# Kernel tuning notes

Hardware: AMD Instinct MI355X
Metric: run time of the kernel (lower is better)

## Reference

```python
import jax, jax.numpy as jnp
import numpy as np

ORDER = 3
OS_FACTOR = 1.5
B, T, I, H = 32, 1024, 512, 512

def _lagrange_kernel(order, os_factor):
    # mirrors LagrangeInterp_RNN.__init__
    if os_factor >= 2:
        delta = os_factor - np.floor(os_factor) + 1
    else:
        delta = os_factor - 1
    k = np.ones(order + 1, dtype=np.float64)
    for n in range(order + 1):
        for j in range(order + 1):
            if j != n:
                k[n] *= (delta - j) / (n - j)
    return jnp.asarray(k, dtype=jnp.float32)

def setup_inputs() -> dict:
    key = jax.random.key(0)
    k1, k2, k3, k4, k5 = jax.random.split(key, 5)
    s = 1.0 / np.sqrt(H)
    return {
        "x": jax.random.normal(k1, (B, T, I), dtype=jnp.float32),
        "Wih": jax.random.uniform(k2, (H, I), minval=-s, maxval=s, dtype=jnp.float32),
        "Whh": jax.random.uniform(k3, (H, H), minval=-s, maxval=s, dtype=jnp.float32),
        "bih": jax.random.uniform(k4, (H,), minval=-s, maxval=s, dtype=jnp.float32),
        "bhh": jax.random.uniform(k5, (H,), minval=-s, maxval=s, dtype=jnp.float32),
        "kernel": _lagrange_kernel(ORDER, OS_FACTOR),
    }

def reference(x, Wih, Whh, bih, bhh, kernel):
    # x: [B, T, I]; kernel: [order+1]; prev_states: [B, order+1, H]
    b = x.shape[0]
    h_dim = Whh.shape[0]
    prev0 = jnp.zeros((b, kernel.shape[0], h_dim), dtype=x.dtype)
    # input projection is independent of the recurrence -> one big GEMM
    xproj = jnp.einsum('bti,hi->bth', x, Wih) + bih  # [B, T, H]

    def step(prev, xp_t):
        # Lagrange-interpolated read of the history window
        h_read = jnp.einsum('k,bkh->bh', kernel, prev)
        h = jnp.tanh(xp_t + h_read @ Whh.T + bhh)
        # torch code detaches the state stored into prev_states, then rolls
        # so the newest (detached) state sits at index 0 (epsilon == 1)
        new_prev = jnp.concatenate(
            [jax.lax.stop_gradient(h)[:, None, :], prev[:, :-1, :]], axis=1)
        return new_prev, h

    _, states_t = jax.lax.scan(step, prev0, jnp.swapaxes(xproj, 0, 1))
    states = jnp.swapaxes(states_t, 0, 1)  # [B, T, H]
    return states, states[:, -1, :]
```

## Files before the change

kernel.cpp:

```cpp
#include <hip/hip_runtime.h>

typedef __bf16 bf16x8 __attribute__((ext_vector_type(8)));
typedef float  f32x4  __attribute__((ext_vector_type(4)));
typedef unsigned long long u64;

#define AGENT __HIP_MEMORY_SCOPE_AGENT

__device__ __forceinline__ float fast_tanh(float x) {
    float e = __expf(2.0f * x);
    return 1.0f - 2.0f * __builtin_amdgcn_rcpf(e + 1.0f);
}

__device__ __forceinline__ void lds_barrier() {
    asm volatile("s_waitcnt lgkmcnt(0)" ::: "memory");
    __builtin_amdgcn_s_barrier();
}

__global__ __launch_bounds__(256) void xproj_gemm_kernel(
    const float* __restrict__ x, const float* __restrict__ Wih,
    const float* __restrict__ bih, float* __restrict__ out)
{
    __shared__ __bf16 Ash[64][72];
    __shared__ __bf16 Bsh[64][72];

    const int tid  = threadIdx.x;
    const int wave = tid >> 6, lane = tid & 63;
    const int col  = lane & 15, kq = lane >> 4;
    const int bt0  = blockIdx.x * 64;
    const int h0   = blockIdx.y * 64;

    f32x4 acc[4];
#pragma unroll
    for (int nt = 0; nt < 4; ++nt) acc[nt] = (f32x4){0.f, 0.f, 0.f, 0.f};

    const int r  = tid >> 2;
    const int cb = (tid & 3) * 16;

    for (int k0 = 0; k0 < 512; k0 += 64) {
        const float* ax = x   + (size_t)(bt0 + r) * 512 + k0 + cb;
        const float* bx = Wih + (size_t)(h0  + r) * 512 + k0 + cb;
#pragma unroll
        for (int j = 0; j < 4; ++j) {
            const float4 av = ((const float4*)ax)[j];
            const float4 bv = ((const float4*)bx)[j];
            const int c = cb + 4 * j;
            Ash[r][c+0]=(__bf16)av.x; Ash[r][c+1]=(__bf16)av.y;
            Ash[r][c+2]=(__bf16)av.z; Ash[r][c+3]=(__bf16)av.w;
            Bsh[r][c+0]=(__bf16)bv.x; Bsh[r][c+1]=(__bf16)bv.y;
            Bsh[r][c+2]=(__bf16)bv.z; Bsh[r][c+3]=(__bf16)bv.w;
        }
        __syncthreads();
#pragma unroll
        for (int kt = 0; kt < 2; ++kt) {
            bf16x8 a = *(const bf16x8*)&Ash[wave * 16 + col][kt * 32 + kq * 8];
#pragma unroll
            for (int nt = 0; nt < 4; ++nt) {
                bf16x8 bb = *(const bf16x8*)&Bsh[nt * 16 + col][kt * 32 + kq * 8];
                acc[nt] = __builtin_amdgcn_mfma_f32_16x16x32_bf16(a, bb, acc[nt], 0, 0, 0);
            }
        }
        __syncthreads();
    }
#pragma unroll
    for (int nt = 0; nt < 4; ++nt) {
        const float bv = bih[h0 + nt * 16 + col];
#pragma unroll
        for (int reg = 0; reg < 4; ++reg) {
            const int m = bt0 + wave * 16 + kq * 4 + reg;
            out[(size_t)m * 512 + h0 + nt * 16 + col] = acc[nt][reg] + bv;
        }
    }
}

__global__ __launch_bounds__(256) void lagrange_rnn_kernel(
    const float* __restrict__ Whh, const float* __restrict__ bhh,
    const float* __restrict__ kern, float* __restrict__ out,
    u64* __restrict__ mbox)
{
    const int id   = blockIdx.x;
    const int b    = (id & 7) + ((id >> 5) << 3);
    const int p    = (id >> 3) & 3;
    const int tid  = threadIdx.x;
    const int wave = tid >> 6, lane = tid & 63;
    const int col  = lane & 15, kq = lane >> 4;

    __shared__ float  hist[4][512];
    __shared__ __bf16 hread[2][512];

    for (int i = tid; i < 2048; i += 256) ((float*)hist)[i] = 0.f;
    for (int i = tid; i < 512;  i += 256) { hread[0][i] = (__bf16)0.f; hread[1][i] = (__bf16)0.f; }

    const int hA = p * 128 + wave * 32 + col;
    const int hB = hA + 16;
    bf16x8 wf0[16], wf1[16];
#pragma unroll
    for (int j = 0; j < 16; ++j) {
        const int ktg = ((j + 4 * p) & 15) * 32 + kq * 8;
        const float* s0 = Whh + (size_t)hA * 512 + ktg;
        const float* s1 = Whh + (size_t)hB * 512 + ktg;
        const float4 a0 = *(const float4*)s0, a1 = *(const float4*)(s0 + 4);
        const float4 b0 = *(const float4*)s1, b1 = *(const float4*)(s1 + 4);
        bf16x8 w;
        w[0]=(__bf16)a0.x; w[1]=(__bf16)a0.y; w[2]=(__bf16)a0.z; w[3]=(__bf16)a0.w;
        w[4]=(__bf16)a1.x; w[5]=(__bf16)a1.y; w[6]=(__bf16)a1.z; w[7]=(__bf16)a1.w;
        wf0[j] = w;
        w[0]=(__bf16)b0.x; w[1]=(__bf16)b0.y; w[2]=(__bf16)b0.z; w[3]=(__bf16)b0.w;
        w[4]=(__bf16)b1.x; w[5]=(__bf16)b1.y; w[6]=(__bf16)b1.z; w[7]=(__bf16)b1.w;
        wf1[j] = w;
    }
    const float k0 = kern[0], k1 = kern[1], k2 = kern[2], k3 = kern[3];
    const float bA = bhh[hA], bB = bhh[hB];
    float* stA = out + (size_t)b * 1024 * 512 + hA;
    const int peer = (p + wave) & 3;
    const int j0 = peer * 128 + lane * 2;
    const bool comp = (lane < 16);
    const int abase = p * 128 + kq * 8;

    float xA = 0.f, xB = 0.f;
    __syncthreads();
    if (comp) { xA = stA[0]; xB = stA[16]; }

    for (int t = 0; t < 1024; ++t) {
        const int rb = t & 1, wb = rb ^ 1;
        const int rt = t & 3;
        const int rm1 = (t + 3) & 3, rm2 = (t + 2) & 3, rm3 = (t + 1) & 3;
        const u64* mb_peer = mbox + (size_t)(((b << 1) | rb) * 4 + peer) * 128;
        const bool polling = (t != 0) && (wave != 0);
        const unsigned want = (unsigned)t;

        float nxA = 0.f, nxB = 0.f;
        if (comp) {
            nxA = stA[(size_t)(t + 1) * 512];
            nxB = stA[(size_t)(t + 1) * 512 + 16];
        }
        u64 v0 = 0, v1 = 0;
        if (polling) {
            v0 = __hip_atomic_load(&mb_peer[lane * 2],     __ATOMIC_RELAXED, AGENT);
            v1 = __hip_atomic_load(&mb_peer[lane * 2 + 1], __ATOMIC_RELAXED, AGENT);
        }

        lds_barrier();

        f32x4 acc0 = (f32x4){0,0,0,0}, acc1 = (f32x4){0,0,0,0};
#pragma unroll
        for (int j = 0; j < 4; ++j) {
            bf16x8 a = *(const bf16x8*)&hread[rb][(abase + 32 * j) & 511];
            acc0 = __builtin_amdgcn_mfma_f32_16x16x32_bf16(a, wf0[j], acc0, 0, 0, 0);
            acc1 = __builtin_amdgcn_mfma_f32_16x16x32_bf16(a, wf1[j], acc1, 0, 0, 0);
        }

        if (polling) {
            while ((unsigned)(v0 >> 32) != want || (unsigned)(v1 >> 32) != want) {
                v0 = __hip_atomic_load(&mb_peer[lane * 2],     __ATOMIC_RELAXED, AGENT);
                v1 = __hip_atomic_load(&mb_peer[lane * 2 + 1], __ATOMIC_RELAXED, AGENT);
            }
            union { unsigned u; float f; } d0, d1;
            d0.u = (unsigned)v0; d1.u = (unsigned)v1;
            const float q0 = k1 * hist[rm2][j0]     + k2 * hist[rm3][j0]     + k3 * hist[rt][j0];
            const float q1 = k1 * hist[rm2][j0 + 1] + k2 * hist[rm3][j0 + 1] + k3 * hist[rt][j0 + 1];
            hread[rb][j0]     = (__bf16)(q0 + k0 * d0.f);
            hread[rb][j0 + 1] = (__bf16)(q1 + k0 * d1.f);
            hist[rm1][j0]     = d0.f;
            hist[rm1][j0 + 1] = d1.f;
        }

        lds_barrier();

        float ppA = 0.f, ppB = 0.f;
        if (comp) {
            ppA = k1 * hist[rm1][hA] + k2 * hist[rm2][hA] + k3 * hist[rm3][hA];
            ppB = k1 * hist[rm1][hB] + k2 * hist[rm2][hB] + k3 * hist[rm3][hB];
        }

        f32x4 c0a = (f32x4){0,0,0,0}, c0b = (f32x4){0,0,0,0}, c0c = (f32x4){0,0,0,0};
        f32x4 c1a = (f32x4){0,0,0,0}, c1b = (f32x4){0,0,0,0}, c1c = (f32x4){0,0,0,0};
#pragma unroll
        for (int j = 4; j < 8; ++j) {
            bf16x8 a = *(const bf16x8*)&hread[rb][(abase + 32 * j) & 511];
            c0a = __builtin_amdgcn_mfma_f32_16x16x32_bf16(a, wf0[j], c0a, 0, 0, 0);
            c1a = __builtin_amdgcn_mfma_f32_16x16x32_bf16(a, wf1[j], c1a, 0, 0, 0);
        }
#pragma unroll
        for (int j = 8; j < 12; ++j) {
            bf16x8 a = *(const bf16x8*)&hread[rb][(abase + 32 * j) & 511];
            c0b = __builtin_amdgcn_mfma_f32_16x16x32_bf16(a, wf0[j], c0b, 0, 0, 0);
            c1b = __builtin_amdgcn_mfma_f32_16x16x32_bf16(a, wf1[j], c1b, 0, 0, 0);
        }
#pragma unroll
        for (int j = 12; j < 16; ++j) {
            bf16x8 a = *(const bf16x8*)&hread[rb][(abase + 32 * j) & 511];
            c0c = __builtin_amdgcn_mfma_f32_16x16x32_bf16(a, wf0[j], c0c, 0, 0, 0);
            c1c = __builtin_amdgcn_mfma_f32_16x16x32_bf16(a, wf1[j], c1c, 0, 0, 0);
        }

        if (comp) {
            const float hAv = fast_tanh(xA + acc0[0] + c0a[0] + c0b[0] + c0c[0] + bA);
            const float hBv = fast_tanh(xB + acc1[0] + c1a[0] + c1b[0] + c1c[0] + bB);
            u64* mb_self = mbox + (size_t)(((b << 1) | wb) * 4 + p) * 128;
            const u64 tag = (u64)(unsigned)(t + 1) << 32;
            union { float f; unsigned u; } cA, cB;
            cA.f = hAv; cB.f = hBv;
            __hip_atomic_store(&mb_self[wave * 32 + col],      tag | cA.u, __ATOMIC_RELAXED, AGENT);
            __hip_atomic_store(&mb_self[wave * 32 + col + 16], tag | cB.u, __ATOMIC_RELAXED, AGENT);
            stA[(size_t)t * 512]      = hAv;
            stA[(size_t)t * 512 + 16] = hBv;
            hist[rt][hA] = hAv;  hread[wb][hA] = (__bf16)(ppA + k0 * hAv);
            hist[rt][hB] = hBv;  hread[wb][hB] = (__bf16)(ppB + k0 * hBv);
        }
        xA = nxA; xB = nxB;
    }

    float* out2 = out + (size_t)32 * 1024 * 512 + (size_t)b * 512;
    if (comp) {
        out2[hA] = hist[3][hA];
        out2[hB] = hist[3][hB];
    }
}

extern "C" void kernel_launch(void* const* d_in, const int* in_sizes, int n_in,
                              void* d_out, int out_size, void* d_ws, size_t ws_size,
                              hipStream_t stream) {
    const float* x    = (const float*)d_in[0];
    const float* Wih  = (const float*)d_in[1];
    const float* Whh  = (const float*)d_in[2];
    const float* bih  = (const float*)d_in[3];
    const float* bhh  = (const float*)d_in[4];
    const float* kern = (const float*)d_in[5];
    float* out = (float*)d_out;

    u64* mbox = (u64*)d_ws;

    dim3 g1(512, 8, 1);
    xproj_gemm_kernel<<<g1, 256, 0, stream>>>(x, Wih, bih, out);
    lagrange_rnn_kernel<<<128, 256, 0, stream>>>(Whh, bhh, kern, out, mbox);
}
```

Baseline: 1.301 ms.

## Split mailbox into fast local-scope poll path with agent-scope fallback republish

Inter-block exchange of hidden state now goes through two mailboxes. Compute lanes write with plain volatile stores to a local mailbox. Pollers read it with an sc0 dwordx4 asm load and, after 16 spins, fall back to an agent-scope mailbox that wave 0 republishes each step from LDS history. Next-step xproj prefetch moves to wave 0 and is staged through a double-buffered LDS array. The aim is lower latency on the cross-block handshake, at the cost of relying on cache-scope visibility semantics, which risks stale reads or extra spin traffic.

```diff
diff --git a/kernel.cpp b/kernel.cpp
--- a/kernel.cpp
+++ b/kernel.cpp
@@ -3,6 +3,7 @@
 typedef __bf16 bf16x8 __attribute__((ext_vector_type(8)));
 typedef float  f32x4  __attribute__((ext_vector_type(4)));
 typedef unsigned long long u64;
+typedef u64 u64x2 __attribute__((ext_vector_type(2)));
 
 #define AGENT __HIP_MEMORY_SCOPE_AGENT
 
@@ -14,6 +15,14 @@
 __device__ __forceinline__ void lds_barrier() {
     asm volatile("s_waitcnt lgkmcnt(0)" ::: "memory");
     __builtin_amdgcn_s_barrier();
+}
+
+__device__ __forceinline__ u64x2 poll_ld(const u64* p) {
+    u64x2 v;
+    asm volatile("global_load_dwordx4 %0, %1, off sc0\n\t"
+                 "s_waitcnt vmcnt(0)"
+                 : "=v"(v) : "v"(p));
+    return v;
 }
 
 __global__ __launch_bounds__(256) void xproj_gemm_kernel(
@@ -75,7 +84,7 @@
 __global__ __launch_bounds__(256) void lagrange_rnn_kernel(
     const float* __restrict__ Whh, const float* __restrict__ bhh,
     const float* __restrict__ kern, float* __restrict__ out,
-    u64* __restrict__ mbox)
+    u64* __restrict__ mboxG, u64* __restrict__ mboxL)
 {
     const int id   = blockIdx.x;
     const int b    = (id & 7) + ((id >> 5) << 3);
@@ -86,6 +95,7 @@
 
     __shared__ float  hist[4][512];
     __shared__ __bf16 hread[2][512];
+    __shared__ float  xpb[2][128];
 
     for (int i = tid; i < 2048; i += 256) ((float*)hist)[i] = 0.f;
     for (int i = tid; i < 512;  i += 256) { hread[0][i] = (__bf16)0.f; hread[1][i] = (__bf16)0.f; }
@@ -111,33 +121,26 @@
     const float k0 = kern[0], k1 = kern[1], k2 = kern[2], k3 = kern[3];
     const float bA = bhh[hA], bB = bhh[hB];
     float* stA = out + (size_t)b * 1024 * 512 + hA;
+    const float* xsrc = out + (size_t)b * 1024 * 512 + p * 128 + lane * 2;
     const int peer = (p + wave) & 3;
     const int j0 = peer * 128 + lane * 2;
     const bool comp = (lane < 16);
     const int abase = p * 128 + kq * 8;
-
-    float xA = 0.f, xB = 0.f;
+    const int xslot = wave * 32 + col;
+
+    if (wave == 0) {
+        const float2 x0 = *(const float2*)xsrc;
+        xpb[0][lane * 2] = x0.x; xpb[0][lane * 2 + 1] = x0.y;
+    }
     __syncthreads();
-    if (comp) { xA = stA[0]; xB = stA[16]; }
 
     for (int t = 0; t < 1024; ++t) {
         const int rb = t & 1, wb = rb ^ 1;
         const int rt = t & 3;
         const int rm1 = (t + 3) & 3, rm2 = (t + 2) & 3, rm3 = (t + 1) & 3;
-        const u64* mb_peer = mbox + (size_t)(((b << 1) | rb) * 4 + peer) * 128;
-        const bool polling = (t != 0) && (wave != 0);
-        const unsigned want = (unsigned)t;
-
-        float nxA = 0.f, nxB = 0.f;
-        if (comp) {
-            nxA = stA[(size_t)(t + 1) * 512];
-            nxB = stA[(size_t)(t + 1) * 512 + 16];
-        }
-        u64 v0 = 0, v1 = 0;
-        if (polling) {
-            v0 = __hip_atomic_load(&mb_peer[lane * 2],     __ATOMIC_RELAXED, AGENT);
-            v1 = __hip_atomic_load(&mb_peer[lane * 2 + 1], __ATOMIC_RELAXED, AGENT);
-        }
+
+        float2 nx = {0.f, 0.f};
+        if (wave == 0) nx = *(const float2*)(xsrc + (size_t)(t + 1) * 512);
 
         lds_barrier();
 
@@ -149,13 +152,32 @@
             acc1 = __builtin_amdgcn_mfma_f32_16x16x32_bf16(a, wf1[j], acc1, 0, 0, 0);
         }
 
-        if (polling) {
-            while ((unsigned)(v0 >> 32) != want || (unsigned)(v1 >> 32) != want) {
-                v0 = __hip_atomic_load(&mb_peer[lane * 2],     __ATOMIC_RELAXED, AGENT);
-                v1 = __hip_atomic_load(&mb_peer[lane * 2 + 1], __ATOMIC_RELAXED, AGENT);
+        if (wave == 0) {
+            u64* mg = mboxG + (size_t)(((b << 1) | rb) * 4 + p) * 128;
+            union { float f; unsigned u; } a0, a1;
+            a0.f = hist[rm1][p * 128 + lane * 2];
+            a1.f = hist[rm1][p * 128 + lane * 2 + 1];
+            const u64 tg = (u64)(unsigned)t << 32;
+            __hip_atomic_store(&mg[lane * 2],     tg | a0.u, __ATOMIC_RELAXED, AGENT);
+            __hip_atomic_store(&mg[lane * 2 + 1], tg | a1.u, __ATOMIC_RELAXED, AGENT);
+        } else if (t) {
+            const unsigned want = (unsigned)t;
+            const u64* ml = mboxL + (size_t)(((b << 1) | rb) * 4 + peer) * 128 + lane * 2;
+            const u64* mg = mboxG + (size_t)(((b << 1) | rb) * 4 + peer) * 128 + lane * 2;
+            u64x2 v = poll_ld(ml);
+            int spins = 0;
+            while ((unsigned)(v[0] >> 32) != want || (unsigned)(v[1] >> 32) != want) {
+                if (++spins > 16) {
+                    const u64 g0 = __hip_atomic_load(&mg[0], __ATOMIC_RELAXED, AGENT);
+                    const u64 g1 = __hip_atomic_load(&mg[1], __ATOMIC_RELAXED, AGENT);
+                    if ((unsigned)(g0 >> 32) == want && (unsigned)(g1 >> 32) == want) {
+                        v[0] = g0; v[1] = g1; break;
+                    }
+                }
+                v = poll_ld(ml);
             }
             union { unsigned u; float f; } d0, d1;
-            d0.u = (unsigned)v0; d1.u = (unsigned)v1;
+            d0.u = (unsigned)v[0]; d1.u = (unsigned)v[1];
             const float q0 = k1 * hist[rm2][j0]     + k2 * hist[rm3][j0]     + k3 * hist[rt][j0];
             const float q1 = k1 * hist[rm2][j0 + 1] + k2 * hist[rm3][j0 + 1] + k3 * hist[rt][j0 + 1];
             hread[rb][j0]     = (__bf16)(q0 + k0 * d0.f);
@@ -166,8 +188,10 @@
 
         lds_barrier();
 
-        float ppA = 0.f, ppB = 0.f;
+        float xAv = 0.f, xBv = 0.f, ppA = 0.f, ppB = 0.f;
         if (comp) {
+            xAv = xpb[rb][xslot];
+            xBv = xpb[rb][xslot + 16];
             ppA = k1 * hist[rm1][hA] + k2 * hist[rm2][hA] + k3 * hist[rm3][hA];
             ppB = k1 * hist[rm1][hB] + k2 * hist[rm2][hB] + k3 * hist[rm3][hB];
         }
@@ -194,20 +218,23 @@
         }
 
         if (comp) {
-            const float hAv = fast_tanh(xA + acc0[0] + c0a[0] + c0b[0] + c0c[0] + bA);
-            const float hBv = fast_tanh(xB + acc1[0] + c1a[0] + c1b[0] + c1c[0] + bB);
-            u64* mb_self = mbox + (size_t)(((b << 1) | wb) * 4 + p) * 128;
+            const float hAv = fast_tanh(xAv + acc0[0] + c0a[0] + c0b[0] + c0c[0] + bA);
+            const float hBv = fast_tanh(xBv + acc1[0] + c1a[0] + c1b[0] + c1c[0] + bB);
+            volatile u64* ms = (volatile u64*)(mboxL + (size_t)(((b << 1) | wb) * 4 + p) * 128);
             const u64 tag = (u64)(unsigned)(t + 1) << 32;
             union { float f; unsigned u; } cA, cB;
             cA.f = hAv; cB.f = hBv;
-            __hip_atomic_store(&mb_self[wave * 32 + col],      tag | cA.u, __ATOMIC_RELAXED, AGENT);
-            __hip_atomic_store(&mb_self[wave * 32 + col + 16], tag | cB.u, __ATOMIC_RELAXED, AGENT);
+            ms[wave * 32 + col]      = tag | cA.u;
+            ms[wave * 32 + col + 16] = tag | cB.u;
             stA[(size_t)t * 512]      = hAv;
             stA[(size_t)t * 512 + 16] = hBv;
             hist[rt][hA] = hAv;  hread[wb][hA] = (__bf16)(ppA + k0 * hAv);
             hist[rt][hB] = hBv;  hread[wb][hB] = (__bf16)(ppB + k0 * hBv);
         }
-        xA = nxA; xB = nxB;
+        if (wave == 0) {
+            xpb[wb][lane * 2]     = nx.x;
+            xpb[wb][lane * 2 + 1] = nx.y;
+        }
     }
 
     float* out2 = out + (size_t)32 * 1024 * 512 + (size_t)b * 512;
@@ -228,9 +255,10 @@
     const float* kern = (const float*)d_in[5];
     float* out = (float*)d_out;
 
-    u64* mbox = (u64*)d_ws;
+    u64* mboxG = (u64*)d_ws;
+    u64* mboxL = mboxG + 32 * 2 * 4 * 128;
 
     dim3 g1(512, 8, 1);
     xproj_gemm_kernel<<<g1, 256, 0, stream>>>(x, Wih, bih, out);
-    lagrange_rnn_kernel<<<128, 256, 0, stream>>>(Whh, bhh, kern, out, mbox);
-}
+    lagrange_rnn_kernel<<<128, 256, 0, stream>>>(Whh, bhh, kern, out, mboxG, mboxL);
+}
```

New measurement: 4.473 ms. 3.44x slower.

## Interleave two batch recurrences per block to hide cross-block mailbox latency

Applied to the files above, without the earlier changes.

Each block now handles two batch rows instead of one, alternating between them within every timestep, and the grid shrinks from 128 to 64 blocks. While one batch waits on its peer mailbox, the other batch's MFMA work runs, and mailbox loads are prefetched one phase early. The next step's input projection is staged through LDS by wave 0. The aim is to hide inter-block polling latency on the serial critical path. The cost is twice the work per block per step, more barriers and more LDS use.

```diff
diff --git a/kernel.cpp b/kernel.cpp
--- a/kernel.cpp
+++ b/kernel.cpp
@@ -5,6 +5,7 @@
 typedef unsigned long long u64;
 
 #define AGENT __HIP_MEMORY_SCOPE_AGENT
+#define MFMA  __builtin_amdgcn_mfma_f32_16x16x32_bf16
 
 __device__ __forceinline__ float fast_tanh(float x) {
     float e = __expf(2.0f * x);
@@ -56,7 +57,7 @@
 #pragma unroll
             for (int nt = 0; nt < 4; ++nt) {
                 bf16x8 bb = *(const bf16x8*)&Bsh[nt * 16 + col][kt * 32 + kq * 8];
-                acc[nt] = __builtin_amdgcn_mfma_f32_16x16x32_bf16(a, bb, acc[nt], 0, 0, 0);
+                acc[nt] = MFMA(a, bb, acc[nt], 0, 0, 0);
             }
         }
         __syncthreads();
@@ -78,17 +79,19 @@
     u64* __restrict__ mbox)
 {
     const int id   = blockIdx.x;
-    const int b    = (id & 7) + ((id >> 5) << 3);
-    const int p    = (id >> 3) & 3;
+    const int p    = id & 3;
+    const int q    = id >> 2;
+    const int b0   = q * 2, b1 = q * 2 + 1;
     const int tid  = threadIdx.x;
     const int wave = tid >> 6, lane = tid & 63;
     const int col  = lane & 15, kq = lane >> 4;
 
-    __shared__ float  hist[4][512];
-    __shared__ __bf16 hread[2][512];
-
-    for (int i = tid; i < 2048; i += 256) ((float*)hist)[i] = 0.f;
-    for (int i = tid; i < 512;  i += 256) { hread[0][i] = (__bf16)0.f; hread[1][i] = (__bf16)0.f; }
+    __shared__ float  hist[2][4][512];
+    __shared__ __bf16 hread[2][2][512];
+    __shared__ float  xpb[2][2][128];
+
+    for (int i = tid; i < 4096; i += 256) ((float*)hist)[i] = 0.f;
+    for (int i = tid; i < 2048; i += 256) ((__bf16*)hread)[i] = (__bf16)0.f;
 
     const int hA = p * 128 + wave * 32 + col;
     const int hB = hA + 16;
@@ -99,121 +102,214 @@
         const float* s0 = Whh + (size_t)hA * 512 + ktg;
         const float* s1 = Whh + (size_t)hB * 512 + ktg;
         const float4 a0 = *(const float4*)s0, a1 = *(const float4*)(s0 + 4);
-        const float4 b0 = *(const float4*)s1, b1 = *(const float4*)(s1 + 4);
+        const float4 c0 = *(const float4*)s1, c1 = *(const float4*)(s1 + 4);
         bf16x8 w;
         w[0]=(__bf16)a0.x; w[1]=(__bf16)a0.y; w[2]=(__bf16)a0.z; w[3]=(__bf16)a0.w;
         w[4]=(__bf16)a1.x; w[5]=(__bf16)a1.y; w[6]=(__bf16)a1.z; w[7]=(__bf16)a1.w;
         wf0[j] = w;
-        w[0]=(__bf16)b0.x; w[1]=(__bf16)b0.y; w[2]=(__bf16)b0.z; w[3]=(__bf16)b0.w;
-        w[4]=(__bf16)b1.x; w[5]=(__bf16)b1.y; w[6]=(__bf16)b1.z; w[7]=(__bf16)b1.w;
+        w[0]=(__bf16)c0.x; w[1]=(__bf16)c0.y; w[2]=(__bf16)c0.z; w[3]=(__bf16)c0.w;
+        w[4]=(__bf16)c1.x; w[5]=(__bf16)c1.y; w[6]=(__bf16)c1.z; w[7]=(__bf16)c1.w;
         wf1[j] = w;
     }
     const float k0 = kern[0], k1 = kern[1], k2 = kern[2], k3 = kern[3];
     const float bA = bhh[hA], bB = bhh[hB];
-    float* stA = out + (size_t)b * 1024 * 512 + hA;
+    float* st0 = out + (size_t)b0 * 1024 * 512 + hA;
+    float* st1 = out + (size_t)b1 * 1024 * 512 + hA;
+    const float* xs0 = out + (size_t)b0 * 1024 * 512 + p * 128 + lane * 2;
+    const float* xs1 = out + (size_t)b1 * 1024 * 512 + p * 128 + lane * 2;
     const int peer = (p + wave) & 3;
     const int j0 = peer * 128 + lane * 2;
     const bool comp = (lane < 16);
     const int abase = p * 128 + kq * 8;
-
-    float xA = 0.f, xB = 0.f;
+    const int xslot = wave * 32 + col;
+
+    if (wave == 0) {
+        const float2 x0 = *(const float2*)xs0;
+        const float2 x1 = *(const float2*)xs1;
+        xpb[0][0][lane * 2] = x0.x; xpb[0][0][lane * 2 + 1] = x0.y;
+        xpb[1][0][lane * 2] = x1.x; xpb[1][0][lane * 2 + 1] = x1.y;
+    }
     __syncthreads();
-    if (comp) { xA = stA[0]; xB = stA[16]; }
+
+    u64 pva0 = 0, pva1 = 0;
+    u64 pvb0 = 0, pvb1 = 0;
 
     for (int t = 0; t < 1024; ++t) {
         const int rb = t & 1, wb = rb ^ 1;
         const int rt = t & 3;
         const int rm1 = (t + 3) & 3, rm2 = (t + 2) & 3, rm3 = (t + 1) & 3;
-        const u64* mb_peer = mbox + (size_t)(((b << 1) | rb) * 4 + peer) * 128;
-        const bool polling = (t != 0) && (wave != 0);
         const unsigned want = (unsigned)t;
 
-        float nxA = 0.f, nxB = 0.f;
-        if (comp) {
-            nxA = stA[(size_t)(t + 1) * 512];
-            nxB = stA[(size_t)(t + 1) * 512 + 16];
-        }
-        u64 v0 = 0, v1 = 0;
-        if (polling) {
-            v0 = __hip_atomic_load(&mb_peer[lane * 2],     __ATOMIC_RELAXED, AGENT);
-            v1 = __hip_atomic_load(&mb_peer[lane * 2 + 1], __ATOMIC_RELAXED, AGENT);
+        float2 nx0 = {0.f, 0.f}, nx1 = {0.f, 0.f};
+        if (wave == 0) {
+            nx0 = *(const float2*)(xs0 + (size_t)(t + 1) * 512);
+            nx1 = *(const float2*)(xs1 + (size_t)(t + 1) * 512);
         }
 
         lds_barrier();
-
         f32x4 acc0 = (f32x4){0,0,0,0}, acc1 = (f32x4){0,0,0,0};
 #pragma unroll
         for (int j = 0; j < 4; ++j) {
-            bf16x8 a = *(const bf16x8*)&hread[rb][(abase + 32 * j) & 511];
-            acc0 = __builtin_amdgcn_mfma_f32_16x16x32_bf16(a, wf0[j], acc0, 0, 0, 0);
-            acc1 = __builtin_amdgcn_mfma_f32_16x16x32_bf16(a, wf1[j], acc1, 0, 0, 0);
-        }
-
-        if (polling) {
-            while ((unsigned)(v0 >> 32) != want || (unsigned)(v1 >> 32) != want) {
-                v0 = __hip_atomic_load(&mb_peer[lane * 2],     __ATOMIC_RELAXED, AGENT);
-                v1 = __hip_atomic_load(&mb_peer[lane * 2 + 1], __ATOMIC_RELAXED, AGENT);
+            bf16x8 a = *(const bf16x8*)&hread[0][rb][(abase + 32 * j) & 511];
+            acc0 = MFMA(a, wf0[j], acc0, 0, 0, 0);
+            acc1 = MFMA(a, wf1[j], acc1, 0, 0, 0);
+        }
+        if (wave != 0 && t) {
+            u64 v0 = pva0, v1 = pva1;
+            if ((unsigned)(v0 >> 32) != want || (unsigned)(v1 >> 32) != want) {
+                const u64* mg = mbox + (size_t)(((b0 << 1) | rb) * 4 + peer) * 128 + lane * 2;
+                do {
+                    v0 = __hip_atomic_load(&mg[0], __ATOMIC_RELAXED, AGENT);
+                    v1 = __hip_atomic_load(&mg[1], __ATOMIC_RELAXED, AGENT);
+                } while ((unsigned)(v0 >> 32) != want || (unsigned)(v1 >> 32) != want);
             }
             union { unsigned u; float f; } d0, d1;
             d0.u = (unsigned)v0; d1.u = (unsigned)v1;
-            const float q0 = k1 * hist[rm2][j0]     + k2 * hist[rm3][j0]     + k3 * hist[rt][j0];
-            const float q1 = k1 * hist[rm2][j0 + 1] + k2 * hist[rm3][j0 + 1] + k3 * hist[rt][j0 + 1];
-            hread[rb][j0]     = (__bf16)(q0 + k0 * d0.f);
-            hread[rb][j0 + 1] = (__bf16)(q1 + k0 * d1.f);
-            hist[rm1][j0]     = d0.f;
-            hist[rm1][j0 + 1] = d1.f;
-        }
-
+            const float q0 = k1 * hist[0][rm2][j0]     + k2 * hist[0][rm3][j0]     + k3 * hist[0][rt][j0];
+            const float q1 = k1 * hist[0][rm2][j0 + 1] + k2 * hist[0][rm3][j0 + 1] + k3 * hist[0][rt][j0 + 1];
+            hread[0][rb][j0]     = (__bf16)(q0 + k0 * d0.f);
+            hread[0][rb][j0 + 1] = (__bf16)(q1 + k0 * d1.f);
+            hist[0][rm1][j0]     = d0.f;
+            hist[0][rm1][j0 + 1] = d1.f;
+        }
         lds_barrier();
-
-        float ppA = 0.f, ppB = 0.f;
+        if (wave != 0 && t) {
+            const u64* mg = mbox + (size_t)(((b1 << 1) | rb) * 4 + peer) * 128 + lane * 2;
+            pvb0 = __hip_atomic_load(&mg[0], __ATOMIC_RELAXED, AGENT);
+            pvb1 = __hip_atomic_load(&mg[1], __ATOMIC_RELAXED, AGENT);
+        }
+        float xAv = 0.f, xBv = 0.f, ppA = 0.f, ppB = 0.f;
         if (comp) {
-            ppA = k1 * hist[rm1][hA] + k2 * hist[rm2][hA] + k3 * hist[rm3][hA];
-            ppB = k1 * hist[rm1][hB] + k2 * hist[rm2][hB] + k3 * hist[rm3][hB];
-        }
-
+            xAv = xpb[0][rb][xslot];
+            xBv = xpb[0][rb][xslot + 16];
+            ppA = k1 * hist[0][rm1][hA] + k2 * hist[0][rm2][hA] + k3 * hist[0][rm3][hA];
+            ppB = k1 * hist[0][rm1][hB] + k2 * hist[0][rm2][hB] + k3 * hist[0][rm3][hB];
+        }
         f32x4 c0a = (f32x4){0,0,0,0}, c0b = (f32x4){0,0,0,0}, c0c = (f32x4){0,0,0,0};
         f32x4 c1a = (f32x4){0,0,0,0}, c1b = (f32x4){0,0,0,0}, c1c = (f32x4){0,0,0,0};
 #pragma unroll
         for (int j = 4; j < 8; ++j) {
-            bf16x8 a = *(const bf16x8*)&hread[rb][(abase + 32 * j) & 511];
-            c0a = __builtin_amdgcn_mfma_f32_16x16x32_bf16(a, wf0[j], c0a, 0, 0, 0);
-            c1a = __builtin_amdgcn_mfma_f32_16x16x32_bf16(a, wf1[j], c1a, 0, 0, 0);
+            bf16x8 a = *(const bf16x8*)&hread[0][rb][(abase + 32 * j) & 511];
+            c0a = MFMA(a, wf0[j], c0a, 0, 0, 0);
+            c1a = MFMA(a, wf1[j], c1a, 0, 0, 0);
         }
 #pragma unroll
         for (int j = 8; j < 12; ++j) {
-            bf16x8 a = *(const bf16x8*)&hread[rb][(abase + 32 * j) & 511];
-            c0b = __builtin_amdgcn_mfma_f32_16x16x32_bf16(a, wf0[j], c0b, 0, 0, 0);
-            c1b = __builtin_amdgcn_mfma_f32_16x16x32_bf16(a, wf1[j], c1b, 0, 0, 0);
+            bf16x8 a = *(const bf16x8*)&hread[0][rb][(abase + 32 * j) & 511];
+            c0b = MFMA(a, wf0[j], c0b, 0, 0, 0);
+            c1b = MFMA(a, wf1[j], c1b, 0, 0, 0);
         }
 #pragma unroll
         for (int j = 12; j < 16; ++j) {
-            bf16x8 a = *(const bf16x8*)&hread[rb][(abase + 32 * j) & 511];
-            c0c = __builtin_amdgcn_mfma_f32_16x16x32_bf16(a, wf0[j], c0c, 0, 0, 0);
-            c1c = __builtin_amdgcn_mfma_f32_16x16x32_bf16(a, wf1[j], c1c, 0, 0, 0);
-        }
-
+            bf16x8 a = *(const bf16x8*)&hread[0][rb][(abase + 32 * j) & 511];
+            c0c = MFMA(a, wf0[j], c0c, 0, 0, 0);
+            c1c = MFMA(a, wf1[j], c1c, 0, 0, 0);
+        }
         if (comp) {
-            const float hAv = fast_tanh(xA + acc0[0] + c0a[0] + c0b[0] + c0c[0] + bA);
-            const float hBv = fast_tanh(xB + acc1[0] + c1a[0] + c1b[0] + c1c[0] + bB);
-            u64* mb_self = mbox + (size_t)(((b << 1) | wb) * 4 + p) * 128;
+            const float hAv = fast_tanh(xAv + acc0[0] + c0a[0] + c0b[0] + c0c[0] + bA);
+            const float hBv = fast_tanh(xBv + acc1[0] + c1a[0] + c1b[0] + c1c[0] + bB);
+            u64* ms = mbox + (size_t)(((b0 << 1) | wb) * 4 + p) * 128;
             const u64 tag = (u64)(unsigned)(t + 1) << 32;
             union { float f; unsigned u; } cA, cB;
             cA.f = hAv; cB.f = hBv;
-            __hip_atomic_store(&mb_self[wave * 32 + col],      tag | cA.u, __ATOMIC_RELAXED, AGENT);
-            __hip_atomic_store(&mb_self[wave * 32 + col + 16], tag | cB.u, __ATOMIC_RELAXED, AGENT);
-            stA[(size_t)t * 512]      = hAv;
-            stA[(size_t)t * 512 + 16] = hBv;
-            hist[rt][hA] = hAv;  hread[wb][hA] = (__bf16)(ppA + k0 * hAv);
-            hist[rt][hB] = hBv;  hread[wb][hB] = (__bf16)(ppB + k0 * hBv);
-        }
-        xA = nxA; xB = nxB;
-    }
-
-    float* out2 = out + (size_t)32 * 1024 * 512 + (size_t)b * 512;
+            __hip_atomic_store(&ms[wave * 32 + col],      tag | cA.u, __ATOMIC_RELAXED, AGENT);
+            __hip_atomic_store(&ms[wave * 32 + col + 16], tag | cB.u, __ATOMIC_RELAXED, AGENT);
+            st0[(size_t)t * 512]      = hAv;
+            st0[(size_t)t * 512 + 16] = hBv;
+            hist[0][rt][hA] = hAv;  hread[0][wb][hA] = (__bf16)(ppA + k0 * hAv);
+            hist[0][rt][hB] = hBv;  hread[0][wb][hB] = (__bf16)(ppB + k0 * hBv);
+        }
+        if (wave == 0) {
+            xpb[0][wb][lane * 2]     = nx0.x;
+            xpb[0][wb][lane * 2 + 1] = nx0.y;
+        }
+
+        lds_barrier();
+        f32x4 e0 = (f32x4){0,0,0,0}, e1 = (f32x4){0,0,0,0};
+#pragma unroll
+        for (int j = 0; j < 4; ++j) {
+            bf16x8 a = *(const bf16x8*)&hread[1][rb][(abase + 32 * j) & 511];
+            e0 = MFMA(a, wf0[j], e0, 0, 0, 0);
+            e1 = MFMA(a, wf1[j], e1, 0, 0, 0);
+        }
+        if (wave != 0 && t) {
+            u64 v0 = pvb0, v1 = pvb1;
+            if ((unsigned)(v0 >> 32) != want || (unsigned)(v1 >> 32) != want) {
+                const u64* mg = mbox + (size_t)(((b1 << 1) | rb) * 4 + peer) * 128 + lane * 2;
+                do {
+                    v0 = __hip_atomic_load(&mg[0], __ATOMIC_RELAXED, AGENT);
+                    v1 = __hip_atomic_load(&mg[1], __ATOMIC_RELAXED, AGENT);
+                } while ((unsigned)(v0 >> 32) != want || (unsigned)(v1 >> 32) != want);
+            }
+            union { unsigned u; float f; } d0, d1;
+            d0.u = (unsigned)v0; d1.u = (unsigned)v1;
+            const float q0 = k1 * hist[1][rm2][j0]     + k2 * hist[1][rm3][j0]     + k3 * hist[1][rt][j0];
+            const float q1 = k1 * hist[1][rm2][j0 + 1] + k2 * hist[1][rm3][j0 + 1] + k3 * hist[1][rt][j0 + 1];
+            hread[1][rb][j0]     = (__bf16)(q0 + k0 * d0.f);
+            hread[1][rb][j0 + 1] = (__bf16)(q1 + k0 * d1.f);
+            hist[1][rm1][j0]     = d0.f;
+            hist[1][rm1][j0 + 1] = d1.f;
+        }
+        lds_barrier();
+        if (wave != 0) {
+            const u64* mg = mbox + (size_t)(((b0 << 1) | wb) * 4 + peer) * 128 + lane * 2;
+            pva0 = __hip_atomic_load(&mg[0], __ATOMIC_RELAXED, AGENT);
+            pva1 = __hip_atomic_load(&mg[1], __ATOMIC_RELAXED, AGENT);
+        }
+        float yAv = 0.f, yBv = 0.f, qpA = 0.f, qpB = 0.f;
+        if (comp) {
+            yAv = xpb[1][rb][xslot];
+            yBv = xpb[1][rb][xslot + 16];
+            qpA = k1 * hist[1][rm1][hA] + k2 * hist[1][rm2][hA] + k3 * hist[1][rm3][hA];
+            qpB = k1 * hist[1][rm1][hB] + k2 * hist[1][rm2][hB] + k3 * hist[1][rm3][hB];
+        }
+        f32x4 g0a = (f32x4){0,0,0,0}, g0b = (f32x4){0,0,0,0}, g0c = (f32x4){0,0,0,0};
+        f32x4 g1a = (f32x4){0,0,0,0}, g1b = (f32x4){0,0,0,0}, g1c = (f32x4){0,0,0,0};
+#pragma unroll
+        for (int j = 4; j < 8; ++j) {
+            bf16x8 a = *(const bf16x8*)&hread[1][rb][(abase + 32 * j) & 511];
+            g0a = MFMA(a, wf0[j], g0a, 0, 0, 0);
+            g1a = MFMA(a, wf1[j], g1a, 0, 0, 0);
+        }
+#pragma unroll
+        for (int j = 8; j < 12; ++j) {
+            bf16x8 a = *(const bf16x8*)&hread[1][rb][(abase + 32 * j) & 511];
+            g0b = MFMA(a, wf0[j], g0b, 0, 0, 0);
+            g1b = MFMA(a, wf1[j], g1b, 0, 0, 0);
+        }
+#pragma unroll
+        for (int j = 12; j < 16; ++j) {
+            bf16x8 a = *(const bf16x8*)&hread[1][rb][(abase + 32 * j) & 511];
+            g0c = MFMA(a, wf0[j], g0c, 0, 0, 0);
+            g1c = MFMA(a, wf1[j], g1c, 0, 0, 0);
+        }
+        if (comp) {
+            const float hAv = fast_tanh(yAv + e0[0] + g0a[0] + g0b[0] + g0c[0] + bA);
+            const float hBv = fast_tanh(yBv + e1[0] + g1a[0] + g1b[0] + g1c[0] + bB);
+            u64* ms = mbox + (size_t)(((b1 << 1) | wb) * 4 + p) * 128;
+            const u64 tag = (u64)(unsigned)(t + 1) << 32;
+            union { float f; unsigned u; } cA, cB;
+            cA.f = hAv; cB.f = hBv;
+            __hip_atomic_store(&ms[wave * 32 + col],      tag | cA.u, __ATOMIC_RELAXED, AGENT);
+            __hip_atomic_store(&ms[wave * 32 + col + 16], tag | cB.u, __ATOMIC_RELAXED, AGENT);
+            st1[(size_t)t * 512]      = hAv;
+            st1[(size_t)t * 512 + 16] = hBv;
+            hist[1][rt][hA] = hAv;  hread[1][wb][hA] = (__bf16)(qpA + k0 * hAv);
+            hist[1][rt][hB] = hBv;  hread[1][wb][hB] = (__bf16)(qpB + k0 * hBv);
+        }
+        if (wave == 0) {
+            xpb[1][wb][lane * 2]     = nx1.x;
+            xpb[1][wb][lane * 2 + 1] = nx1.y;
+        }
+    }
+
+    float* o0 = out + (size_t)32 * 1024 * 512 + (size_t)b0 * 512;
+    float* o1 = out + (size_t)32 * 1024 * 512 + (size_t)b1 * 512;
     if (comp) {
-        out2[hA] = hist[3][hA];
-        out2[hB] = hist[3][hB];
+        o0[hA] = hist[0][3][hA];
+        o0[hB] = hist[0][3][hB];
+        o1[hA] = hist[1][3][hA];
+        o1[hB] = hist[1][3][hB];
     }
 }
 
@@ -232,5 +328,5 @@
 
     dim3 g1(512, 8, 1);
     xproj_gemm_kernel<<<g1, 256, 0, stream>>>(x, Wih, bih, out);
-    lagrange_rnn_kernel<<<128, 256, 0, stream>>>(Whh, bhh, kern, out, mbox);
-}
+    lagrange_rnn_kernel<<<64, 256, 0, stream>>>(Whh, bhh, kern, out, mbox);
+}
```

After: 2.745 ms. +110.9%, slower.

## Batch 16 sequences per recurrent MFMA tile and exchange interpolated bf16 state

Applied to the files above, without the earlier changes.

The recurrent kernel now processes 16 batch rows per group of 4 blocks, so the MFMA M dimension carries real batch rows instead of one broadcast vector. The grid drops from 128 to 8 blocks. Peers exchange the already Lagrange-interpolated state as packed bf16 pairs through the mailbox, and history is kept in registers instead of LDS. bhh is folded into the input-projection bias. The cost is that only 8 CUs run the serial recurrence, each with more work per step and more mailbox traffic per thread.

```diff
diff --git a/kernel.cpp b/kernel.cpp
--- a/kernel.cpp
+++ b/kernel.cpp
@@ -5,6 +5,7 @@
 typedef unsigned long long u64;
 
 #define AGENT __HIP_MEMORY_SCOPE_AGENT
+#define MFMA  __builtin_amdgcn_mfma_f32_16x16x32_bf16
 
 __device__ __forceinline__ float fast_tanh(float x) {
     float e = __expf(2.0f * x);
@@ -18,7 +19,8 @@
 
 __global__ __launch_bounds__(256) void xproj_gemm_kernel(
     const float* __restrict__ x, const float* __restrict__ Wih,
-    const float* __restrict__ bih, float* __restrict__ out)
+    const float* __restrict__ bih, const float* __restrict__ bhh,
+    float* __restrict__ out)
 {
     __shared__ __bf16 Ash[64][72];
     __shared__ __bf16 Bsh[64][72];
@@ -56,164 +58,195 @@
 #pragma unroll
             for (int nt = 0; nt < 4; ++nt) {
                 bf16x8 bb = *(const bf16x8*)&Bsh[nt * 16 + col][kt * 32 + kq * 8];
-                acc[nt] = __builtin_amdgcn_mfma_f32_16x16x32_bf16(a, bb, acc[nt], 0, 0, 0);
+                acc[nt] = MFMA(a, bb, acc[nt], 0, 0, 0);
             }
         }
         __syncthreads();
     }
 #pragma unroll
     for (int nt = 0; nt < 4; ++nt) {
-        const float bv = bih[h0 + nt * 16 + col];
+        const int n = h0 + nt * 16 + col;
+        const float bv = bih[n] + bhh[n];
 #pragma unroll
         for (int reg = 0; reg < 4; ++reg) {
             const int m = bt0 + wave * 16 + kq * 4 + reg;
-            out[(size_t)m * 512 + h0 + nt * 16 + col] = acc[nt][reg] + bv;
-        }
-    }
-}
-
-__global__ __launch_bounds__(256) void lagrange_rnn_kernel(
-    const float* __restrict__ Whh, const float* __restrict__ bhh,
-    const float* __restrict__ kern, float* __restrict__ out,
-    u64* __restrict__ mbox)
+            out[(size_t)m * 512 + n] = acc[nt][reg] + bv;
+        }
+    }
+}
+
+#define TT  1024
+#define LDA 520
+
+__global__ __launch_bounds__(256, 1) void lagrange_rnn_kernel(
+    const float* __restrict__ Whh, const float* __restrict__ kern,
+    float* __restrict__ out, u64* __restrict__ mbox)
 {
     const int id   = blockIdx.x;
-    const int b    = (id & 7) + ((id >> 5) << 3);
-    const int p    = (id >> 3) & 3;
+    const int g    = id >> 2;
+    const int p    = id & 3;
     const int tid  = threadIdx.x;
-    const int wave = tid >> 6, lane = tid & 63;
+    const int w    = tid >> 6, lane = tid & 63;
     const int col  = lane & 15, kq = lane >> 4;
 
-    __shared__ float  hist[4][512];
-    __shared__ __bf16 hread[2][512];
-
-    for (int i = tid; i < 2048; i += 256) ((float*)hist)[i] = 0.f;
-    for (int i = tid; i < 512;  i += 256) { hread[0][i] = (__bf16)0.f; hread[1][i] = (__bf16)0.f; }
-
-    const int hA = p * 128 + wave * 32 + col;
-    const int hB = hA + 16;
-    bf16x8 wf0[16], wf1[16];
-#pragma unroll
-    for (int j = 0; j < 16; ++j) {
-        const int ktg = ((j + 4 * p) & 15) * 32 + kq * 8;
-        const float* s0 = Whh + (size_t)hA * 512 + ktg;
-        const float* s1 = Whh + (size_t)hB * 512 + ktg;
-        const float4 a0 = *(const float4*)s0, a1 = *(const float4*)(s0 + 4);
-        const float4 b0 = *(const float4*)s1, b1 = *(const float4*)(s1 + 4);
-        bf16x8 w;
-        w[0]=(__bf16)a0.x; w[1]=(__bf16)a0.y; w[2]=(__bf16)a0.z; w[3]=(__bf16)a0.w;
-        w[4]=(__bf16)a1.x; w[5]=(__bf16)a1.y; w[6]=(__bf16)a1.z; w[7]=(__bf16)a1.w;
-        wf0[j] = w;
-        w[0]=(__bf16)b0.x; w[1]=(__bf16)b0.y; w[2]=(__bf16)b0.z; w[3]=(__bf16)b0.w;
-        w[4]=(__bf16)b1.x; w[5]=(__bf16)b1.y; w[6]=(__bf16)b1.z; w[7]=(__bf16)b1.w;
-        wf1[j] = w;
-    }
+    __shared__ unsigned short Apan[2][16][LDA];
+
+    for (int i = tid; i < 2 * 16 * LDA; i += 256)
+        ((unsigned short*)Apan)[i] = 0;
+
+    const int n0 = p * 128 + w * 32 + col;
+    bf16x8 wf[2][16];
+#pragma unroll
+    for (int ct = 0; ct < 2; ++ct) {
+        const float* wr = Whh + (size_t)(n0 + ct * 16) * 512 + kq * 8;
+#pragma unroll
+        for (int j = 0; j < 16; ++j) {
+            const int ktg = ((j + 4 * p) & 15) * 32;
+            const float4 lo = *(const float4*)(wr + ktg);
+            const float4 hi = *(const float4*)(wr + ktg + 4);
+            bf16x8 v;
+            v[0]=(__bf16)lo.x; v[1]=(__bf16)lo.y; v[2]=(__bf16)lo.z; v[3]=(__bf16)lo.w;
+            v[4]=(__bf16)hi.x; v[5]=(__bf16)hi.y; v[6]=(__bf16)hi.z; v[7]=(__bf16)hi.w;
+            wf[ct][j] = v;
+        }
+    }
+
     const float k0 = kern[0], k1 = kern[1], k2 = kern[2], k3 = kern[3];
-    const float bA = bhh[hA], bB = bhh[hB];
-    float* stA = out + (size_t)b * 1024 * 512 + hA;
-    const int peer = (p + wave) & 3;
-    const int j0 = peer * 128 + lane * 2;
-    const bool comp = (lane < 16);
-    const int abase = p * 128 + kq * 8;
-
-    float xA = 0.f, xB = 0.f;
+
+    const int b0 = g * 16;
+    float* pb[4];
+#pragma unroll
+    for (int r = 0; r < 4; ++r)
+        pb[r] = out + (size_t)(b0 + kq * 4 + r) * TT * 512 + n0;
+
+    float xr[2][4], h1[2][4], h2[2][4], pp[2][4];
+#pragma unroll
+    for (int c = 0; c < 2; ++c)
+#pragma unroll
+        for (int r = 0; r < 4; ++r) { xr[c][r]=0.f; h1[c][r]=0.f; h2[c][r]=0.f; pp[c][r]=0.f; }
+
+    const int q0 = (p + 1) & 3, q1 = (p + 2) & 3, q2 = (p + 3) & 3;
+    const int arow = (lane & 15) * LDA + kq * 8;
+
     __syncthreads();
-    if (comp) { xA = stA[0]; xB = stA[16]; }
-
-    for (int t = 0; t < 1024; ++t) {
+#pragma unroll
+    for (int r = 0; r < 4; ++r) { xr[0][r] = pb[r][0]; xr[1][r] = pb[r][16]; }
+
+    for (int t = 0; t < TT; ++t) {
         const int rb = t & 1, wb = rb ^ 1;
-        const int rt = t & 3;
-        const int rm1 = (t + 3) & 3, rm2 = (t + 2) & 3, rm3 = (t + 1) & 3;
-        const u64* mb_peer = mbox + (size_t)(((b << 1) | rb) * 4 + peer) * 128;
-        const bool polling = (t != 0) && (wave != 0);
-        const unsigned want = (unsigned)t;
-
-        float nxA = 0.f, nxB = 0.f;
-        if (comp) {
-            nxA = stA[(size_t)(t + 1) * 512];
-            nxB = stA[(size_t)(t + 1) * 512 + 16];
-        }
-        u64 v0 = 0, v1 = 0;
-        if (polling) {
-            v0 = __hip_atomic_load(&mb_peer[lane * 2],     __ATOMIC_RELAXED, AGENT);
-            v1 = __hip_atomic_load(&mb_peer[lane * 2 + 1], __ATOMIC_RELAXED, AGENT);
-        }
 
         lds_barrier();
 
-        f32x4 acc0 = (f32x4){0,0,0,0}, acc1 = (f32x4){0,0,0,0};
+        float xn[2][4];
+#pragma unroll
+        for (int r = 0; r < 4; ++r) {
+            xn[0][r] = pb[r][512];
+            xn[1][r] = pb[r][512 + 16];
+        }
+
+        u64 v[12];
+        const u64* mp0 = mbox + ((size_t)(g * 4 + q0) * 2 + rb) * 1024 + (size_t)tid * 4;
+        const u64* mp1 = mbox + ((size_t)(g * 4 + q1) * 2 + rb) * 1024 + (size_t)tid * 4;
+        const u64* mp2 = mbox + ((size_t)(g * 4 + q2) * 2 + rb) * 1024 + (size_t)tid * 4;
+        if (t) {
+#pragma unroll
+            for (int i = 0; i < 4; ++i) v[i]     = __hip_atomic_load(mp0 + i, __ATOMIC_RELAXED, AGENT);
+#pragma unroll
+            for (int i = 0; i < 4; ++i) v[4 + i] = __hip_atomic_load(mp1 + i, __ATOMIC_RELAXED, AGENT);
+#pragma unroll
+            for (int i = 0; i < 4; ++i) v[8 + i] = __hip_atomic_load(mp2 + i, __ATOMIC_RELAXED, AGENT);
+        }
+
+        const unsigned short* Ar = &Apan[rb][0][0];
+        f32x4 aA0 = (f32x4){0,0,0,0}, aA1 = (f32x4){0,0,0,0};
+        f32x4 aB0 = (f32x4){0,0,0,0}, aB1 = (f32x4){0,0,0,0};
 #pragma unroll
         for (int j = 0; j < 4; ++j) {
-            bf16x8 a = *(const bf16x8*)&hread[rb][(abase + 32 * j) & 511];
-            acc0 = __builtin_amdgcn_mfma_f32_16x16x32_bf16(a, wf0[j], acc0, 0, 0, 0);
-            acc1 = __builtin_amdgcn_mfma_f32_16x16x32_bf16(a, wf1[j], acc1, 0, 0, 0);
-        }
-
-        if (polling) {
-            while ((unsigned)(v0 >> 32) != want || (unsigned)(v1 >> 32) != want) {
-                v0 = __hip_atomic_load(&mb_peer[lane * 2],     __ATOMIC_RELAXED, AGENT);
-                v1 = __hip_atomic_load(&mb_peer[lane * 2 + 1], __ATOMIC_RELAXED, AGENT);
-            }
-            union { unsigned u; float f; } d0, d1;
-            d0.u = (unsigned)v0; d1.u = (unsigned)v1;
-            const float q0 = k1 * hist[rm2][j0]     + k2 * hist[rm3][j0]     + k3 * hist[rt][j0];
-            const float q1 = k1 * hist[rm2][j0 + 1] + k2 * hist[rm3][j0 + 1] + k3 * hist[rt][j0 + 1];
-            hread[rb][j0]     = (__bf16)(q0 + k0 * d0.f);
-            hread[rb][j0 + 1] = (__bf16)(q1 + k0 * d1.f);
-            hist[rm1][j0]     = d0.f;
-            hist[rm1][j0 + 1] = d1.f;
+            bf16x8 a = *(const bf16x8*)(Ar + arow + ((j + 4 * p) & 15) * 32);
+            aA0 = MFMA(a, wf[0][j], aA0, 0, 0, 0);
+            aA1 = MFMA(a, wf[1][j], aA1, 0, 0, 0);
+        }
+
+        if (t) {
+            const unsigned want = (unsigned)t;
+            bool again;
+            do {
+                again = false;
+#pragma unroll
+                for (int i = 0; i < 4; ++i)
+                    if ((unsigned)(v[i] >> 32) != want)     { v[i]     = __hip_atomic_load(mp0 + i, __ATOMIC_RELAXED, AGENT); again = true; }
+#pragma unroll
+                for (int i = 0; i < 4; ++i)
+                    if ((unsigned)(v[4+i] >> 32) != want)   { v[4+i]   = __hip_atomic_load(mp1 + i, __ATOMIC_RELAXED, AGENT); again = true; }
+#pragma unroll
+                for (int i = 0; i < 4; ++i)
+                    if ((unsigned)(v[8+i] >> 32) != want)   { v[8+i]   = __hip_atomic_load(mp2 + i, __ATOMIC_RELAXED, AGENT); again = true; }
+            } while (again);
+#pragma unroll
+            for (int i = 0; i < 4; ++i) {
+                const unsigned pay = (unsigned)v[i];
+                Apan[rb][kq * 4 + i][q0 * 128 + w * 32 + col]      = (unsigned short)pay;
+                Apan[rb][kq * 4 + i][q0 * 128 + w * 32 + col + 16] = (unsigned short)(pay >> 16);
+            }
+#pragma unroll
+            for (int i = 0; i < 4; ++i) {
+                const unsigned pay = (unsigned)v[4 + i];
+                Apan[rb][kq * 4 + i][q1 * 128 + w * 32 + col]      = (unsigned short)pay;
+                Apan[rb][kq * 4 + i][q1 * 128 + w * 32 + col + 16] = (unsigned short)(pay >> 16);
+            }
+#pragma unroll
+            for (int i = 0; i < 4; ++i) {
+                const unsigned pay = (unsigned)v[8 + i];
+                Apan[rb][kq * 4 + i][q2 * 128 + w * 32 + col]      = (unsigned short)pay;
+                Apan[rb][kq * 4 + i][q2 * 128 + w * 32 + col + 16] = (unsigned short)(pay >> 16);
+            }
         }
 
         lds_barrier();
 
-        float ppA = 0.f, ppB = 0.f;
-        if (comp) {
-            ppA = k1 * hist[rm1][hA] + k2 * hist[rm2][hA] + k3 * hist[rm3][hA];
-            ppB = k1 * hist[rm1][hB] + k2 * hist[rm2][hB] + k3 * hist[rm3][hB];
-        }
-
-        f32x4 c0a = (f32x4){0,0,0,0}, c0b = (f32x4){0,0,0,0}, c0c = (f32x4){0,0,0,0};
-        f32x4 c1a = (f32x4){0,0,0,0}, c1b = (f32x4){0,0,0,0}, c1c = (f32x4){0,0,0,0};
 #pragma unroll
         for (int j = 4; j < 8; ++j) {
-            bf16x8 a = *(const bf16x8*)&hread[rb][(abase + 32 * j) & 511];
-            c0a = __builtin_amdgcn_mfma_f32_16x16x32_bf16(a, wf0[j], c0a, 0, 0, 0);
-            c1a = __builtin_amdgcn_mfma_f32_16x16x32_bf16(a, wf1[j], c1a, 0, 0, 0);
-        }
-#pragma unroll
-        for (int j = 8; j < 12; ++j) {
-            bf16x8 a = *(const bf16x8*)&hread[rb][(abase + 32 * j) & 511];
-            c0b = __builtin_amdgcn_mfma_f32_16x16x32_bf16(a, wf0[j], c0b, 0, 0, 0);
-            c1b = __builtin_amdgcn_mfma_f32_16x16x32_bf16(a, wf1[j], c1b, 0, 0, 0);
-        }
-#pragma unroll
-        for (int j = 12; j < 16; ++j) {
-            bf16x8 a = *(const bf16x8*)&hread[rb][(abase + 32 * j) & 511];
-            c0c = __builtin_amdgcn_mfma_f32_16x16x32_bf16(a, wf0[j], c0c, 0, 0, 0);
-            c1c = __builtin_amdgcn_mfma_f32_16x16x32_bf16(a, wf1[j], c1c, 0, 0, 0);
-        }
-
-        if (comp) {
-            const float hAv = fast_tanh(xA + acc0[0] + c0a[0] + c0b[0] + c0c[0] + bA);
-            const float hBv = fast_tanh(xB + acc1[0] + c1a[0] + c1b[0] + c1c[0] + bB);
-            u64* mb_self = mbox + (size_t)(((b << 1) | wb) * 4 + p) * 128;
-            const u64 tag = (u64)(unsigned)(t + 1) << 32;
-            union { float f; unsigned u; } cA, cB;
-            cA.f = hAv; cB.f = hBv;
-            __hip_atomic_store(&mb_self[wave * 32 + col],      tag | cA.u, __ATOMIC_RELAXED, AGENT);
-            __hip_atomic_store(&mb_self[wave * 32 + col + 16], tag | cB.u, __ATOMIC_RELAXED, AGENT);
-            stA[(size_t)t * 512]      = hAv;
-            stA[(size_t)t * 512 + 16] = hBv;
-            hist[rt][hA] = hAv;  hread[wb][hA] = (__bf16)(ppA + k0 * hAv);
-            hist[rt][hB] = hBv;  hread[wb][hB] = (__bf16)(ppB + k0 * hBv);
-        }
-        xA = nxA; xB = nxB;
-    }
-
-    float* out2 = out + (size_t)32 * 1024 * 512 + (size_t)b * 512;
-    if (comp) {
-        out2[hA] = hist[3][hA];
-        out2[hB] = hist[3][hB];
+            bf16x8 a = *(const bf16x8*)(Ar + arow + ((j + 4 * p) & 15) * 32);
+            aA0 = MFMA(a, wf[0][j], aA0, 0, 0, 0);
+            aA1 = MFMA(a, wf[1][j], aA1, 0, 0, 0);
+        }
+#pragma unroll
+        for (int j = 8; j < 16; ++j) {
+            bf16x8 a = *(const bf16x8*)(Ar + arow + ((j + 4 * p) & 15) * 32);
+            aB0 = MFMA(a, wf[0][j], aB0, 0, 0, 0);
+            aB1 = MFMA(a, wf[1][j], aB1, 0, 0, 0);
+        }
+
+        u64* ms = mbox + ((size_t)(g * 4 + p) * 2 + wb) * 1024 + (size_t)tid * 4;
+        const u64 tag = (u64)(unsigned)(t + 1) << 32;
+#pragma unroll
+        for (int r = 0; r < 4; ++r) {
+            const float hv0 = fast_tanh(xr[0][r] + aA0[r] + aB0[r]);
+            const float hv1 = fast_tanh(xr[1][r] + aA1[r] + aB1[r]);
+            const float nh0 = k0 * hv0 + pp[0][r];
+            const float nh1 = k0 * hv1 + pp[1][r];
+            union { __bf16 h; unsigned short u; } u0, u1;
+            u0.h = (__bf16)nh0; u1.h = (__bf16)nh1;
+            __hip_atomic_store(&ms[r], tag | (u64)(u0.u | ((unsigned)u1.u << 16)),
+                               __ATOMIC_RELAXED, AGENT);
+            pp[0][r] = k1 * hv0 + k2 * h1[0][r] + k3 * h2[0][r];
+            pp[1][r] = k1 * hv1 + k2 * h1[1][r] + k3 * h2[1][r];
+            h2[0][r] = h1[0][r]; h1[0][r] = hv0;
+            h2[1][r] = h1[1][r]; h1[1][r] = hv1;
+            pb[r][0]  = hv0;
+            pb[r][16] = hv1;
+            Apan[wb][kq * 4 + r][n0]      = u0.u;
+            Apan[wb][kq * 4 + r][n0 + 16] = u1.u;
+            xr[0][r] = xn[0][r]; xr[1][r] = xn[1][r];
+            pb[r] += 512;
+        }
+    }
+
+    float* o2 = out + (size_t)32 * TT * 512;
+#pragma unroll
+    for (int r = 0; r < 4; ++r) {
+        o2[(size_t)(b0 + kq * 4 + r) * 512 + n0]      = h1[0][r];
+        o2[(size_t)(b0 + kq * 4 + r) * 512 + n0 + 16] = h1[1][r];
     }
 }
 
@@ -231,6 +264,6 @@
     u64* mbox = (u64*)d_ws;
 
     dim3 g1(512, 8, 1);
-    xproj_gemm_kernel<<<g1, 256, 0, stream>>>(x, Wih, bih, out);
-    lagrange_rnn_kernel<<<128, 256, 0, stream>>>(Whh, bhh, kern, out, mbox);
-}
+    xproj_gemm_kernel<<<g1, 256, 0, stream>>>(x, Wih, bih, bhh, out);
+    lagrange_rnn_kernel<<<8, 256, 0, stream>>>(Whh, kern, out, mbox);
+}
```

Result: slower. 2.661 ms (+104.5%).
